# Kernel optimization log

Measured on AMD Instinct MI355X. Metric: run time of the kernel, lower is better.

Reference implementation:

```python
import jax, jax.numpy as jnp
import numpy as np

T, B = 2048, 128
H = 128          # hidden_size
QH = 1024        # query_hidden_size
NF = 32          # num_convolution_filters
K = 31           # convolution_filter_size (odd, same padding)


def setup_inputs() -> dict:
    key = jax.random.key(0)
    ks = jax.random.split(key, 10)
    encoded_tokens = jax.random.normal(ks[0], (T, B, H), dtype=jnp.float32)
    tokens_mask = jax.random.randint(ks[1], (B, T), 0, 2).astype(jnp.bool_)
    query = jax.random.normal(ks[2], (1, B, QH), dtype=jnp.float32)
    cumulative_alignment = jax.random.uniform(ks[3], (B, T), dtype=jnp.float32)
    # parameters
    conv_w = jax.random.normal(ks[4], (NF, 1, K), dtype=jnp.float32) * 0.1   # Conv1d weight [out,in,k]
    conv_b = jnp.zeros((NF,), dtype=jnp.float32)
    Wq = jax.random.normal(ks[5], (H, QH), dtype=jnp.float32) * (1.0 / np.sqrt(QH))
    bq = jnp.zeros((H,), dtype=jnp.float32)
    Wa = jax.random.normal(ks[6], (H, NF), dtype=jnp.float32) * (1.0 / np.sqrt(NF))
    ba = jnp.zeros((H,), dtype=jnp.float32)
    score_w = jax.random.normal(ks[7], (H,), dtype=jnp.float32) * (1.0 / np.sqrt(H))  # xavier-ish
    score_b = jnp.zeros((H,), dtype=jnp.float32)
    return dict(encoded_tokens=encoded_tokens, tokens_mask=tokens_mask, query=query,
                cumulative_alignment=cumulative_alignment, conv_w=conv_w, conv_b=conv_b,
                Wq=Wq, bq=bq, Wa=Wa, ba=ba, score_w=score_w, score_b=score_b)


def reference(encoded_tokens, tokens_mask, query, cumulative_alignment,
              conv_w, conv_b, Wq, bq, Wa, ba, score_w, score_b):
    # location features: Conv1d over cumulative alignment, same padding
    loc = jax.lax.conv_general_dilated(
        cumulative_alignment[:, None, :], conv_w,
        window_strides=(1,), padding=[((K - 1) // 2, (K - 1) // 2)],
        dimension_numbers=('NCH', 'OIH', 'NCH'))  # [B, NF, T]
    loc = loc + conv_b[None, :, None]
    loc = jnp.transpose(loc, (2, 0, 1))                        # [T, B, NF]
    loc = jnp.einsum('tbf,hf->tbh', loc, Wa) + ba              # [T, B, H]
    q = jnp.einsum('obq,hq->obh', query, Wq) + bq              # [1, B, H]
    # additive score: tanh of fused elementwise sum, then project to scalar
    score = jnp.tanh(encoded_tokens + q + loc + score_b)       # [T, B, H]
    s = jnp.einsum('tbh,h->bt', score, score_w)                # [B, T]
    s = jnp.where(tokens_mask, -jnp.inf, s)
    alignment = jax.nn.softmax(s, axis=1)                      # [B, T]
    context = jnp.einsum('bt,tbh->bh', alignment, encoded_tokens)  # [B, H]
    cumulative_alignment = cumulative_alignment + alignment
    return context, cumulative_alignment, alignment
```

## Files before the change

### kernel.cpp

```cpp
#include <hip/hip_runtime.h>
#include <stdint.h>

#define T_DIM 2048
#define B_DIM 128
#define H_DIM 128
#define QH_DIM 1024
#define NF 32
#define KW 31
#define TT 32
#define TW 8

__device__ __forceinline__ float fast_tanh(float x) {
    float e = __expf(2.0f * x);
    return 1.0f - 2.0f * __builtin_amdgcn_rcpf(1.0f + e);
}

__device__ __forceinline__ float rfl(float x) {
    return __uint_as_float(__builtin_amdgcn_readfirstlane(__float_as_uint(x)));
}

__global__ void k0_G(const float* __restrict__ Wa, const float* __restrict__ conv_w,
                     float* __restrict__ G) {
    int gid = blockIdx.x * blockDim.x + threadIdx.x;
    if (gid >= H_DIM * KW) return;
    int k = gid >> 7, h = gid & 127;
    float acc = 0.0f;
    #pragma unroll
    for (int f = 0; f < NF; ++f) acc = fmaf(Wa[h * NF + f], conv_w[f * KW + k], acc);
    G[gid] = acc;
}

__global__ __launch_bounds__(512)
void k1_query(const float* __restrict__ query, const float* __restrict__ Wq,
              const float* __restrict__ bq, const float* __restrict__ Wa,
              const float* __restrict__ conv_b, const float* __restrict__ ba,
              const float* __restrict__ score_b, float* __restrict__ qb) {
    const int b = blockIdx.x, tid = threadIdx.x;
    const int h = tid & 127, qtr = tid >> 7;
    __shared__ __align__(16) float qrow[QH_DIM];
    __shared__ float partial[512];
    for (int i = tid; i < QH_DIM; i += 512) qrow[i] = query[b * QH_DIM + i];
    __syncthreads();
    const float4* wq4 = (const float4*)(Wq + (size_t)h * QH_DIM + qtr * 256);
    const float4* q4 = (const float4*)(qrow + qtr * 256);
    float acc = 0.0f;
    #pragma unroll 4
    for (int j = 0; j < 64; ++j) {
        float4 w = wq4[j], q = q4[j];
        acc += w.x * q.x + w.y * q.y + w.z * q.z + w.w * q.w;
    }
    if (qtr == 0) {
        float cb = bq[h] + ba[h] + score_b[h];
        #pragma unroll
        for (int f = 0; f < NF; ++f) cb = fmaf(Wa[h * NF + f], conv_b[f], cb);
        acc += cb;
    }
    partial[tid] = acc;
    __syncthreads();
    if (tid < 128) qb[b * H_DIM + h] = partial[h] + partial[h + 128] + partial[h + 256] + partial[h + 384];
}

__global__ __launch_bounds__(256, 4)
void k2_score(const float* __restrict__ enc, const float* __restrict__ cum,
              const float* __restrict__ G, const float* __restrict__ qb,
              const float* __restrict__ score_w, float* __restrict__ s_out) {
    const int b = blockIdx.y;
    const int t0 = blockIdx.x * TT;
    const int tid = threadIdx.x;
    const int l = tid & 63, wv = tid >> 6;

    __shared__ float Gs[KW * H_DIM];
    __shared__ float cw[TT + KW - 1];

    #pragma unroll
    for (int i = tid; i < KW * H_DIM; i += 256) Gs[i] = G[i];
    if (tid < TT + KW - 1) {
        int t = t0 - (KW / 2) + tid;
        cw[tid] = (t >= 0 && t < T_DIM) ? cum[b * T_DIM + t] : 0.0f;
    }
    __syncthreads();

    float sc[TW + KW - 1];
    #pragma unroll
    for (int j = 0; j < TW + KW - 1; ++j) sc[j] = rfl(cw[wv * TW + j]);

    const float2 base = *(const float2*)(qb + b * H_DIM + 2 * l);
    const float2 w2 = *(const float2*)(score_w + 2 * l);

    const int tw0 = t0 + wv * TW;
    const float* ep0 = enc + ((size_t)tw0 * B_DIM + b) * H_DIM + 2 * l;

    float2 acc[TW];
    #pragma unroll
    for (int it = 0; it < TW; ++it) {
        const float2 e = *(const float2*)(ep0 + (size_t)it * (B_DIM * H_DIM));
        acc[it].x = base.x + e.x;
        acc[it].y = base.y + e.y;
    }

    {
        float2 g[16];
        #pragma unroll
        for (int kk = 0; kk < 16; ++kk) g[kk] = *(const float2*)(&Gs[kk * H_DIM + 2 * l]);
        #pragma unroll
        for (int kk = 0; kk < 16; ++kk) {
            #pragma unroll
            for (int it = 0; it < TW; ++it) {
                const float c = sc[it + kk];
                acc[it].x = fmaf(g[kk].x, c, acc[it].x);
                acc[it].y = fmaf(g[kk].y, c, acc[it].y);
            }
        }
    }
    {
        float2 g[15];
        #pragma unroll
        for (int kk = 0; kk < 15; ++kk) g[kk] = *(const float2*)(&Gs[(16 + kk) * H_DIM + 2 * l]);
        #pragma unroll
        for (int kk = 0; kk < 15; ++kk) {
            #pragma unroll
            for (int it = 0; it < TW; ++it) {
                const float c = sc[it + 16 + kk];
                acc[it].x = fmaf(g[kk].x, c, acc[it].x);
                acc[it].y = fmaf(g[kk].y, c, acc[it].y);
            }
        }
    }

    #pragma unroll
    for (int it = 0; it < TW; ++it) {
        float p = w2.x * fast_tanh(acc[it].x) + w2.y * fast_tanh(acc[it].y);
        #pragma unroll
        for (int m = 32; m >= 1; m >>= 1) p += __shfl_xor(p, m, 64);
        if (l == 0) s_out[b * T_DIM + tw0 + it] = p;
    }
}

__global__ __launch_bounds__(256)
void k3_softmax(float* __restrict__ s_align, const void* __restrict__ mask,
                const float* __restrict__ cum_in, float* __restrict__ cum_out) {
    const int b = blockIdx.x, tid = threadIdx.x;
    const int wave = tid >> 6, lane = tid & 63;

    uint32_t u = ((const uint32_t*)mask)[lane];
    unsigned long long hi = __ballot(u > 1u);
    unsigned long long nf = __ballot(u != 0u && u != 0x3f800000u);
    int layout = (hi == 0ull) ? 0 : ((nf == 0ull) ? 2 : 1);

    float v[8];
    float mx = -__builtin_inff();
    #pragma unroll
    for (int i = 0; i < 8; ++i) {
        int idx = b * T_DIM + tid + i * 256;
        bool m;
        if (layout == 0)      m = ((const int32_t*)mask)[idx] != 0;
        else if (layout == 1) m = ((const uint8_t*)mask)[idx] != 0;
        else                  m = ((const float*)mask)[idx] != 0.0f;
        v[i] = m ? -__builtin_inff() : s_align[idx];
        mx = fmaxf(mx, v[i]);
    }
    #pragma unroll
    for (int s = 32; s >= 1; s >>= 1) mx = fmaxf(mx, __shfl_xor(mx, s, 64));
    __shared__ float redm[4], reds[4];
    if (lane == 0) redm[wave] = mx;
    __syncthreads();
    mx = fmaxf(fmaxf(redm[0], redm[1]), fmaxf(redm[2], redm[3]));

    float e[8], sum = 0.0f;
    #pragma unroll
    for (int i = 0; i < 8; ++i) { e[i] = __expf(v[i] - mx); sum += e[i]; }
    #pragma unroll
    for (int s = 32; s >= 1; s >>= 1) sum += __shfl_xor(sum, s, 64);
    if (lane == 0) reds[wave] = sum;
    __syncthreads();
    sum = reds[0] + reds[1] + reds[2] + reds[3];
    const float inv = 1.0f / sum;

    #pragma unroll
    for (int i = 0; i < 8; ++i) {
        int idx = b * T_DIM + tid + i * 256;
        float a = e[i] * inv;
        s_align[idx] = a;
        cum_out[idx] = cum_in[idx] + a;
    }
}

__global__ __launch_bounds__(256)
void k4_context(const float* __restrict__ enc, const float* __restrict__ align,
                float* __restrict__ ctx) {
    const int b = blockIdx.y, t0 = blockIdx.x * 128;
    const int tid = threadIdx.x;
    const int q = tid & 31, r = tid >> 5;
    __shared__ float al[128];
    if (tid < 128) al[tid] = align[b * T_DIM + t0 + tid];
    __syncthreads();
    const float* ep = enc + ((size_t)(t0 + r) * B_DIM + b) * H_DIM + 4 * q;
    float4 acc = {0.0f, 0.0f, 0.0f, 0.0f};
    #pragma unroll
    for (int i = 0; i < 16; ++i) {
        const float a = al[r + 8 * i];
        const float4 v = *(const float4*)(ep + (size_t)(8 * i) * (B_DIM * H_DIM));
        acc.x = fmaf(a, v.x, acc.x);
        acc.y = fmaf(a, v.y, acc.y);
        acc.z = fmaf(a, v.z, acc.z);
        acc.w = fmaf(a, v.w, acc.w);
    }
    __shared__ float4 part[8][32];
    part[r][q] = acc;
    __syncthreads();
    if (tid < 32) {
        float4 s = part[0][q];
        #pragma unroll
        for (int rr = 1; rr < 8; ++rr) {
            float4 p = part[rr][q];
            s.x += p.x; s.y += p.y; s.z += p.z; s.w += p.w;
        }
        float* dst = ctx + b * H_DIM + 4 * q;
        atomicAdd(dst + 0, s.x);
        atomicAdd(dst + 1, s.y);
        atomicAdd(dst + 2, s.z);
        atomicAdd(dst + 3, s.w);
    }
}

extern "C" void kernel_launch(void* const* d_in, const int* in_sizes, int n_in,
                              void* d_out, int out_size, void* d_ws, size_t ws_size,
                              hipStream_t stream) {
    const float* enc     = (const float*)d_in[0];
    const void*  mask    = d_in[1];
    const float* query   = (const float*)d_in[2];
    const float* cum     = (const float*)d_in[3];
    const float* conv_w  = (const float*)d_in[4];
    const float* conv_b  = (const float*)d_in[5];
    const float* Wq      = (const float*)d_in[6];
    const float* bq      = (const float*)d_in[7];
    const float* Wa      = (const float*)d_in[8];
    const float* ba      = (const float*)d_in[9];
    const float* score_w = (const float*)d_in[10];
    const float* score_b = (const float*)d_in[11];

    float* ctx_out   = (float*)d_out;
    float* cum_out   = ctx_out + B_DIM * H_DIM;
    float* align_out = cum_out + B_DIM * T_DIM;

    float* G  = (float*)d_ws;
    float* qb = G + 4096;

    hipMemsetAsync(ctx_out, 0, B_DIM * H_DIM * sizeof(float), stream);
    k0_G<<<16, 256, 0, stream>>>(Wa, conv_w, G);
    k1_query<<<B_DIM, 512, 0, stream>>>(query, Wq, bq, Wa, conv_b, ba, score_b, qb);
    k2_score<<<dim3(T_DIM / TT, B_DIM), 256, 0, stream>>>(enc, cum, G, qb, score_w, align_out);
    k3_softmax<<<B_DIM, 256, 0, stream>>>(align_out, mask, cum, cum_out);
    k4_context<<<dim3(16, B_DIM), 256, 0, stream>>>(enc, align_out, ctx_out);
}
```

Before: 284.8 us.

## Fuse score, masked online softmax and context into one pass over encoder

Merges the score, softmax and context kernels into a flash-style kernel. Each block computes scores for a 128-step tile, applies the mask, and keeps a running max, sum and exp-weighted context from the encoder values it has already loaded. A small final kernel combines the per-tile partials into the context and normalized alignment. This removes the second full read of the encoder tensor, the atomics and the memset, at the cost of extra exp work and more work per block. The grid is also reordered so batch is the fast index and tiles are made larger.

```diff
diff --git a/kernel.cpp b/kernel.cpp
--- a/kernel.cpp
+++ b/kernel.cpp
@@ -7,16 +7,14 @@
 #define QH_DIM 1024
 #define NF 32
 #define KW 31
-#define TT 32
-#define TW 8
+#define TT 128
+#define NTILE (T_DIM / TT)
+
+#define NEG_INF (-__builtin_inff())
 
 __device__ __forceinline__ float fast_tanh(float x) {
     float e = __expf(2.0f * x);
     return 1.0f - 2.0f * __builtin_amdgcn_rcpf(1.0f + e);
-}
-
-__device__ __forceinline__ float rfl(float x) {
-    return __uint_as_float(__builtin_amdgcn_readfirstlane(__float_as_uint(x)));
 }
 
 __global__ void k0_G(const float* __restrict__ Wa, const float* __restrict__ conv_w,
@@ -62,17 +60,36 @@
 
 __global__ __launch_bounds__(256, 4)
 void k2_score(const float* __restrict__ enc, const float* __restrict__ cum,
-              const float* __restrict__ G, const float* __restrict__ qb,
-              const float* __restrict__ score_w, float* __restrict__ s_out) {
-    const int b = blockIdx.y;
-    const int t0 = blockIdx.x * TT;
+              const void* __restrict__ mask, const float* __restrict__ G,
+              const float* __restrict__ qb, const float* __restrict__ score_w,
+              float* __restrict__ s_out, float* __restrict__ o_part,
+              float* __restrict__ ml_part) {
+    const int b = blockIdx.x;
+    const int tile = blockIdx.y;
+    const int t0 = tile * TT;
     const int tid = threadIdx.x;
     const int l = tid & 63, wv = tid >> 6;
 
     __shared__ float Gs[KW * H_DIM];
     __shared__ float cw[TT + KW - 1];
-
-    #pragma unroll
+    __shared__ float mbias[TT];
+    __shared__ float oc[4][H_DIM];
+    __shared__ float mwl[4], lwl[4];
+
+    {
+        uint32_t u = ((const uint32_t*)mask)[l];
+        unsigned long long hi = __ballot(u > 1u);
+        unsigned long long nf = __ballot(u != 0u && u != 0x3f800000u);
+        int layout = (hi == 0ull) ? 0 : ((nf == 0ull) ? 2 : 1);
+        if (tid < TT) {
+            int idx = b * T_DIM + t0 + tid;
+            bool m;
+            if (layout == 0)      m = ((const int32_t*)mask)[idx] != 0;
+            else if (layout == 1) m = ((const uint8_t*)mask)[idx] != 0;
+            else                  m = ((const float*)mask)[idx] != 0.0f;
+            mbias[tid] = m ? NEG_INF : 0.0f;
+        }
+    }
     for (int i = tid; i < KW * H_DIM; i += 256) Gs[i] = G[i];
     if (tid < TT + KW - 1) {
         int t = t0 - (KW / 2) + tid;
@@ -80,146 +97,137 @@
     }
     __syncthreads();
 
-    float sc[TW + KW - 1];
-    #pragma unroll
-    for (int j = 0; j < TW + KW - 1; ++j) sc[j] = rfl(cw[wv * TW + j]);
-
     const float2 base = *(const float2*)(qb + b * H_DIM + 2 * l);
     const float2 w2 = *(const float2*)(score_w + 2 * l);
 
-    const int tw0 = t0 + wv * TW;
-    const float* ep0 = enc + ((size_t)tw0 * B_DIM + b) * H_DIM + 2 * l;
-
-    float2 acc[TW];
-    #pragma unroll
-    for (int it = 0; it < TW; ++it) {
-        const float2 e = *(const float2*)(ep0 + (size_t)it * (B_DIM * H_DIM));
-        acc[it].x = base.x + e.x;
-        acc[it].y = base.y + e.y;
-    }
-
-    {
-        float2 g[16];
-        #pragma unroll
-        for (int kk = 0; kk < 16; ++kk) g[kk] = *(const float2*)(&Gs[kk * H_DIM + 2 * l]);
-        #pragma unroll
-        for (int kk = 0; kk < 16; ++kk) {
-            #pragma unroll
-            for (int it = 0; it < TW; ++it) {
-                const float c = sc[it + kk];
-                acc[it].x = fmaf(g[kk].x, c, acc[it].x);
-                acc[it].y = fmaf(g[kk].y, c, acc[it].y);
+    float m_w = NEG_INF, l_w = 0.0f;
+    float ox = 0.0f, oy = 0.0f;
+
+    #pragma unroll
+    for (int si = 0; si < 4; ++si) {
+        const int cbase = wv * 32 + si * 8;
+        float2 acc[8];
+        #pragma unroll
+        for (int it = 0; it < 8; ++it) acc[it] = base;
+
+        {
+            float tp[23];
+            #pragma unroll
+            for (int j = 0; j < 23; ++j) tp[j] = cw[cbase + j];
+            #pragma unroll
+            for (int k = 0; k < 16; ++k) {
+                const float2 gk = *(const float2*)(&Gs[k * H_DIM + 2 * l]);
+                #pragma unroll
+                for (int it = 0; it < 8; ++it) {
+                    acc[it].x = fmaf(gk.x, tp[k + it], acc[it].x);
+                    acc[it].y = fmaf(gk.y, tp[k + it], acc[it].y);
+                }
             }
         }
-    }
-    {
-        float2 g[15];
-        #pragma unroll
-        for (int kk = 0; kk < 15; ++kk) g[kk] = *(const float2*)(&Gs[(16 + kk) * H_DIM + 2 * l]);
-        #pragma unroll
-        for (int kk = 0; kk < 15; ++kk) {
-            #pragma unroll
-            for (int it = 0; it < TW; ++it) {
-                const float c = sc[it + 16 + kk];
-                acc[it].x = fmaf(g[kk].x, c, acc[it].x);
-                acc[it].y = fmaf(g[kk].y, c, acc[it].y);
+        {
+            float tp[22];
+            #pragma unroll
+            for (int j = 0; j < 22; ++j) tp[j] = cw[cbase + 16 + j];
+            #pragma unroll
+            for (int k = 16; k < 31; ++k) {
+                const float2 gk = *(const float2*)(&Gs[k * H_DIM + 2 * l]);
+                #pragma unroll
+                for (int it = 0; it < 8; ++it) {
+                    acc[it].x = fmaf(gk.x, tp[k - 16 + it], acc[it].x);
+                    acc[it].y = fmaf(gk.y, tp[k - 16 + it], acc[it].y);
+                }
             }
         }
-    }
-
-    #pragma unroll
-    for (int it = 0; it < TW; ++it) {
-        float p = w2.x * fast_tanh(acc[it].x) + w2.y * fast_tanh(acc[it].y);
-        #pragma unroll
-        for (int m = 32; m >= 1; m >>= 1) p += __shfl_xor(p, m, 64);
-        if (l == 0) s_out[b * T_DIM + tw0 + it] = p;
+
+        const float* ep = enc + ((size_t)(t0 + cbase) * B_DIM + b) * H_DIM + 2 * l;
+        float ex[8], ey[8], s_arr[8];
+        #pragma unroll
+        for (int it = 0; it < 8; ++it) {
+            const float2 e2 = *(const float2*)(ep + (size_t)it * (B_DIM * H_DIM));
+            ex[it] = e2.x; ey[it] = e2.y;
+            float p = w2.x * fast_tanh(acc[it].x + e2.x)
+                    + w2.y * fast_tanh(acc[it].y + e2.y);
+            #pragma unroll
+            for (int m = 32; m >= 1; m >>= 1) p += __shfl_xor(p, m, 64);
+            s_arr[it] = p + mbias[cbase + it];
+        }
+        float sv = s_arr[0];
+        #pragma unroll
+        for (int it = 1; it < 8; ++it) sv = (l == it) ? s_arr[it] : sv;
+        if (l < 8) s_out[b * T_DIM + t0 + cbase + l] = sv;
+        float m8 = s_arr[0];
+        #pragma unroll
+        for (int it = 1; it < 8; ++it) m8 = fmaxf(m8, s_arr[it]);
+        const float m_new = fmaxf(m_w, m8);
+        const float m_use = (m_new == NEG_INF) ? 0.0f : m_new;
+        const float alpha = __expf(m_w - m_use);
+        float lsum = 0.0f, osx = 0.0f, osy = 0.0f;
+        #pragma unroll
+        for (int it = 0; it < 8; ++it) {
+            const float e = __expf(s_arr[it] - m_use);
+            lsum += e;
+            osx = fmaf(e, ex[it], osx);
+            osy = fmaf(e, ey[it], osy);
+        }
+        l_w = fmaf(l_w, alpha, lsum);
+        ox = fmaf(ox, alpha, osx);
+        oy = fmaf(oy, alpha, osy);
+        m_w = m_new;
+    }
+
+    oc[wv][2 * l] = ox;
+    oc[wv][2 * l + 1] = oy;
+    if (l == 0) { mwl[wv] = m_w; lwl[wv] = l_w; }
+    __syncthreads();
+    if (tid < H_DIM) {
+        const float mb = fmaxf(fmaxf(mwl[0], mwl[1]), fmaxf(mwl[2], mwl[3]));
+        const float mu = (mb == NEG_INF) ? 0.0f : mb;
+        const float b0 = __expf(mwl[0] - mu), b1 = __expf(mwl[1] - mu);
+        const float b2 = __expf(mwl[2] - mu), b3 = __expf(mwl[3] - mu);
+        const float o = oc[0][tid] * b0 + oc[1][tid] * b1 + oc[2][tid] * b2 + oc[3][tid] * b3;
+        const int tbase = b * NTILE + tile;
+        o_part[tbase * H_DIM + tid] = o;
+        if (tid == 0) {
+            ml_part[tbase * 2] = mb;
+            ml_part[tbase * 2 + 1] = lwl[0] * b0 + lwl[1] * b1 + lwl[2] * b2 + lwl[3] * b3;
+        }
     }
 }
 
 __global__ __launch_bounds__(256)
-void k3_softmax(float* __restrict__ s_align, const void* __restrict__ mask,
-                const float* __restrict__ cum_in, float* __restrict__ cum_out) {
+void k5_final(float* __restrict__ s_align, const float* __restrict__ cum_in,
+              float* __restrict__ cum_out, const float* __restrict__ o_part,
+              const float* __restrict__ ml_part, float* __restrict__ ctx) {
     const int b = blockIdx.x, tid = threadIdx.x;
-    const int wave = tid >> 6, lane = tid & 63;
-
-    uint32_t u = ((const uint32_t*)mask)[lane];
-    unsigned long long hi = __ballot(u > 1u);
-    unsigned long long nf = __ballot(u != 0u && u != 0x3f800000u);
-    int layout = (hi == 0ull) ? 0 : ((nf == 0ull) ? 2 : 1);
-
-    float v[8];
-    float mx = -__builtin_inff();
-    #pragma unroll
-    for (int i = 0; i < 8; ++i) {
-        int idx = b * T_DIM + tid + i * 256;
-        bool m;
-        if (layout == 0)      m = ((const int32_t*)mask)[idx] != 0;
-        else if (layout == 1) m = ((const uint8_t*)mask)[idx] != 0;
-        else                  m = ((const float*)mask)[idx] != 0.0f;
-        v[i] = m ? -__builtin_inff() : s_align[idx];
-        mx = fmaxf(mx, v[i]);
-    }
-    #pragma unroll
-    for (int s = 32; s >= 1; s >>= 1) mx = fmaxf(mx, __shfl_xor(mx, s, 64));
-    __shared__ float redm[4], reds[4];
-    if (lane == 0) redm[wave] = mx;
-    __syncthreads();
-    mx = fmaxf(fmaxf(redm[0], redm[1]), fmaxf(redm[2], redm[3]));
-
-    float e[8], sum = 0.0f;
-    #pragma unroll
-    for (int i = 0; i < 8; ++i) { e[i] = __expf(v[i] - mx); sum += e[i]; }
-    #pragma unroll
-    for (int s = 32; s >= 1; s >>= 1) sum += __shfl_xor(sum, s, 64);
-    if (lane == 0) reds[wave] = sum;
-    __syncthreads();
-    sum = reds[0] + reds[1] + reds[2] + reds[3];
-    const float inv = 1.0f / sum;
-
-    #pragma unroll
-    for (int i = 0; i < 8; ++i) {
-        int idx = b * T_DIM + tid + i * 256;
-        float a = e[i] * inv;
+    __shared__ float sm[NTILE], sl[NTILE], sb[NTILE];
+    if (tid < NTILE) {
+        sm[tid] = ml_part[(b * NTILE + tid) * 2];
+        sl[tid] = ml_part[(b * NTILE + tid) * 2 + 1];
+    }
+    __syncthreads();
+    float M = sm[0];
+    #pragma unroll
+    for (int i = 1; i < NTILE; ++i) M = fmaxf(M, sm[i]);
+    const float M_use = (M == NEG_INF) ? 0.0f : M;
+    if (tid < NTILE) sb[tid] = __expf(sm[tid] - M_use);
+    __syncthreads();
+    float L = 0.0f;
+    #pragma unroll
+    for (int i = 0; i < NTILE; ++i) L = fmaf(sl[i], sb[i], L);
+    const float invL = 1.0f / L;
+    if (tid < H_DIM) {
+        float o = 0.0f;
+        #pragma unroll
+        for (int i = 0; i < NTILE; ++i)
+            o = fmaf(o_part[(b * NTILE + i) * H_DIM + tid], sb[i], o);
+        ctx[b * H_DIM + tid] = o * invL;
+    }
+    #pragma unroll
+    for (int j = 0; j < 8; ++j) {
+        const int idx = b * T_DIM + tid + j * 256;
+        const float a = __expf(s_align[idx] - M_use) * invL;
         s_align[idx] = a;
         cum_out[idx] = cum_in[idx] + a;
-    }
-}
-
-__global__ __launch_bounds__(256)
-void k4_context(const float* __restrict__ enc, const float* __restrict__ align,
-                float* __restrict__ ctx) {
-    const int b = blockIdx.y, t0 = blockIdx.x * 128;
-    const int tid = threadIdx.x;
-    const int q = tid & 31, r = tid >> 5;
-    __shared__ float al[128];
-    if (tid < 128) al[tid] = align[b * T_DIM + t0 + tid];
-    __syncthreads();
-    const float* ep = enc + ((size_t)(t0 + r) * B_DIM + b) * H_DIM + 4 * q;
-    float4 acc = {0.0f, 0.0f, 0.0f, 0.0f};
-    #pragma unroll
-    for (int i = 0; i < 16; ++i) {
-        const float a = al[r + 8 * i];
-        const float4 v = *(const float4*)(ep + (size_t)(8 * i) * (B_DIM * H_DIM));
-        acc.x = fmaf(a, v.x, acc.x);
-        acc.y = fmaf(a, v.y, acc.y);
-        acc.z = fmaf(a, v.z, acc.z);
-        acc.w = fmaf(a, v.w, acc.w);
-    }
-    __shared__ float4 part[8][32];
-    part[r][q] = acc;
-    __syncthreads();
-    if (tid < 32) {
-        float4 s = part[0][q];
-        #pragma unroll
-        for (int rr = 1; rr < 8; ++rr) {
-            float4 p = part[rr][q];
-            s.x += p.x; s.y += p.y; s.z += p.z; s.w += p.w;
-        }
-        float* dst = ctx + b * H_DIM + 4 * q;
-        atomicAdd(dst + 0, s.x);
-        atomicAdd(dst + 1, s.y);
-        atomicAdd(dst + 2, s.z);
-        atomicAdd(dst + 3, s.w);
     }
 }
 
@@ -243,13 +251,14 @@
     float* cum_out   = ctx_out + B_DIM * H_DIM;
     float* align_out = cum_out + B_DIM * T_DIM;
 
-    float* G  = (float*)d_ws;
-    float* qb = G + 4096;
-
-    hipMemsetAsync(ctx_out, 0, B_DIM * H_DIM * sizeof(float), stream);
+    float* G      = (float*)d_ws;
+    float* qb     = G + 4096;
+    float* o_part = qb + B_DIM * H_DIM;
+    float* ml     = o_part + B_DIM * NTILE * H_DIM;
+
     k0_G<<<16, 256, 0, stream>>>(Wa, conv_w, G);
     k1_query<<<B_DIM, 512, 0, stream>>>(query, Wq, bq, Wa, conv_b, ba, score_b, qb);
-    k2_score<<<dim3(T_DIM / TT, B_DIM), 256, 0, stream>>>(enc, cum, G, qb, score_w, align_out);
-    k3_softmax<<<B_DIM, 256, 0, stream>>>(align_out, mask, cum, cum_out);
-    k4_context<<<dim3(16, B_DIM), 256, 0, stream>>>(enc, align_out, ctx_out);
-}
+    k2_score<<<dim3(B_DIM, NTILE), 256, 0, stream>>>(enc, cum, mask, G, qb, score_w,
+                                                     align_out, o_part, ml);
+    k5_final<<<B_DIM, 256, 0, stream>>>(align_out, cum, cum_out, o_part, ml, ctx_out);
+}
```

Result: faster. 262.7 us (-7.8%).
